# Kernel tuning notes

Hardware: AMD Instinct MI355X
Metric: run time of the kernel (lower is better)

## Reference

```python
import jax, jax.numpy as jnp
import numpy as np

N_NODES = 100000


def gcn_conv(x, edge_index, W, b, num_nodes):
    """PyG GCNConv: y = D^{-1/2} (A + I) D^{-1/2} (x W) + b.

    edge_index[0] = source (row), edge_index[1] = target (col);
    messages flow source -> target with symmetric normalization.
    """
    # add self loops
    loop = jnp.arange(num_nodes, dtype=edge_index.dtype)
    row = jnp.concatenate([edge_index[0], loop])  # [E+N]
    col = jnp.concatenate([edge_index[1], loop])  # [E+N]

    xw = x @ W  # [N, F_out] -- tiny GEMM, done before gather

    # degree of target nodes (incl. self loops)
    ones = jnp.ones(col.shape[0], dtype=x.dtype)
    deg = jax.ops.segment_sum(ones, col, num_segments=num_nodes)  # [N]
    dis = jax.lax.rsqrt(jnp.maximum(deg, 1e-12))
    dis = jnp.where(deg > 0, dis, 0.0)

    norm = dis[row] * dis[col]  # [E+N]
    msg = xw[row] * norm[:, None]  # gather + scale, [E+N, F_out]
    out = jax.ops.segment_sum(msg, col, num_segments=num_nodes)  # scatter-add
    return out + b


def setup_inputs() -> dict:
    key = jax.random.key(0)
    k1, k2, k3, k4 = jax.random.split(key, 4)
    num_attr, hidden, num_classes = 128, 16, 8
    n_edges = 3200000
    x = jax.random.normal(k1, (N_NODES, num_attr), dtype=jnp.float32)
    edge_index = jax.random.randint(k2, (2, n_edges), 0, N_NODES, dtype=jnp.int64)
    W1 = jax.random.normal(k3, (num_attr, hidden), dtype=jnp.float32) / np.sqrt(num_attr)
    b1 = jnp.zeros((hidden,), dtype=jnp.float32)
    W2 = jax.random.normal(k4, (hidden, num_classes), dtype=jnp.float32) / np.sqrt(hidden)
    b2 = jnp.zeros((num_classes,), dtype=jnp.float32)
    return {"x": x, "edge_index": edge_index, "W1": W1, "b1": b1, "W2": W2, "b2": b2}


def reference(x, edge_index, W1, b1, W2, b2):
    h = gcn_conv(x, edge_index, W1, b1, N_NODES)
    h = jax.nn.relu(h)
    # dropout is identity in eval mode
    h = gcn_conv(h, edge_index, W2, b2, N_NODES)
    return jax.nn.sigmoid(h)  # [N, num_classes]
```

## Files before the change

### kernel.cpp

```cpp
#include <hip/hip_runtime.h>
#include <math.h>

static constexpr int FI = 128;
static constexpr int FH = 16;
static constexpr int FO = 8;

static constexpr int BIN_SHIFT = 8;
static constexpr int BIN_NODES = 256;
static constexpr int MAX_BINS  = 512;
static constexpr int CAPB      = 8832;
static constexpr int SCHUNK    = 4096;
static constexpr int SThreads  = 512;

__device__ __forceinline__ unsigned short f2bf(float x) {
    unsigned u = __float_as_uint(x);
    u += 0x7FFFu + ((u >> 16) & 1u);
    return (unsigned short)(u >> 16);
}
__device__ __forceinline__ float bflo(unsigned u) { return __uint_as_float(u << 16); }
__device__ __forceinline__ float bfhi(unsigned u) { return __uint_as_float(u & 0xFFFF0000u); }

struct SMemScatter {
    int lcnt[MAX_BINS];
    int lstart[MAX_BINS];
    int lcur[MAX_BINS];
    int gbase[MAX_BINS];
    int wsum[8];
    unsigned int   staged[SCHUNK];
    unsigned short sbin[SCHUNK];
};
struct SMemGemm { float sw[FI * FH]; };
union SMemU { SMemScatter s; SMemGemm g; };

__launch_bounds__(SThreads)
__global__ void k_scatter_gemm(const int* __restrict__ row, const int* __restrict__ col,
                               int* __restrict__ binCursor, unsigned int* __restrict__ binned,
                               const float* __restrict__ x, const float* __restrict__ W1,
                               unsigned short* __restrict__ xw1, int E, int nchunks, int N) {
    __shared__ SMemU sm;
    int t = threadIdx.x;

    if ((int)blockIdx.x >= nchunks) {
        for (int i = t; i < FI * FH; i += SThreads) sm.g.sw[i] = W1[i];
        __syncthreads();
        int nl = t >> 2;
        int f  = (t & 3) * 4;
        int n  = ((int)blockIdx.x - nchunks) * 128 + nl;
        if (n >= N) return;
        const float4* xr = (const float4*)(x + (size_t)n * FI);
        float a0 = 0.f, a1 = 0.f, a2 = 0.f, a3 = 0.f;
        #pragma unroll 8
        for (int kq = 0; kq < FI / 4; ++kq) {
            float4 xv = xr[kq];
            float4 w0 = *(const float4*)&sm.g.sw[(kq * 4 + 0) * FH + f];
            float4 w1 = *(const float4*)&sm.g.sw[(kq * 4 + 1) * FH + f];
            float4 w2 = *(const float4*)&sm.g.sw[(kq * 4 + 2) * FH + f];
            float4 w3 = *(const float4*)&sm.g.sw[(kq * 4 + 3) * FH + f];
            a0 = fmaf(xv.x, w0.x, a0); a1 = fmaf(xv.x, w0.y, a1);
            a2 = fmaf(xv.x, w0.z, a2); a3 = fmaf(xv.x, w0.w, a3);
            a0 = fmaf(xv.y, w1.x, a0); a1 = fmaf(xv.y, w1.y, a1);
            a2 = fmaf(xv.y, w1.z, a2); a3 = fmaf(xv.y, w1.w, a3);
            a0 = fmaf(xv.z, w2.x, a0); a1 = fmaf(xv.z, w2.y, a1);
            a2 = fmaf(xv.z, w2.z, a2); a3 = fmaf(xv.z, w2.w, a3);
            a0 = fmaf(xv.w, w3.x, a0); a1 = fmaf(xv.w, w3.y, a1);
            a2 = fmaf(xv.w, w3.z, a2); a3 = fmaf(xv.w, w3.w, a3);
        }
        unsigned w0 = (unsigned)f2bf(a0) | ((unsigned)f2bf(a1) << 16);
        unsigned w1 = (unsigned)f2bf(a2) | ((unsigned)f2bf(a3) << 16);
        *(uint2*)(xw1 + (size_t)n * FH + f) = make_uint2(w0, w1);
        return;
    }

    int base = blockIdx.x * SCHUNK;
    int end  = base + SCHUNK; if (end > E) end = E;
    int m = end - base;
    sm.s.lcnt[t] = 0;
    __syncthreads();

    int nv = m >> 2;
    const int4* c4 = (const int4*)(col + base);
    int4 creg[2];
    #pragma unroll
    for (int j = 0; j < 2; ++j) {
        int k = t + j * SThreads;
        if (k < nv) {
            creg[j] = c4[k];
            atomicAdd(&sm.s.lcnt[creg[j].x >> BIN_SHIFT], 1);
            atomicAdd(&sm.s.lcnt[creg[j].y >> BIN_SHIFT], 1);
            atomicAdd(&sm.s.lcnt[creg[j].z >> BIN_SHIFT], 1);
            atomicAdd(&sm.s.lcnt[creg[j].w >> BIN_SHIFT], 1);
        }
    }
    for (int i = base + (nv << 2) + t; i < end; i += SThreads)
        atomicAdd(&sm.s.lcnt[col[i] >> BIN_SHIFT], 1);
    __syncthreads();

    int v = sm.s.lcnt[t];
    int inc = v;
    #pragma unroll
    for (int d = 1; d < 64; d <<= 1) {
        int u = __shfl_up(inc, d, 64);
        if ((t & 63) >= d) inc += u;
    }
    if ((t & 63) == 63) sm.s.wsum[t >> 6] = inc;
    __syncthreads();
    if (t < 8) {
        int w = sm.s.wsum[t];
        #pragma unroll
        for (int d = 1; d < 8; d <<= 1) {
            int u = __shfl_up(w, d, 8);
            if (t >= d) w += u;
        }
        sm.s.wsum[t] = w;
    }
    __syncthreads();
    {
        int waveoff = (t >= 64) ? sm.s.wsum[(t >> 6) - 1] : 0;
        int ex = waveoff + inc - v;
        sm.s.lstart[t] = ex;
        sm.s.lcur[t]   = ex;
        sm.s.gbase[t]  = v ? atomicAdd(&binCursor[t], v) : 0;
    }
    __syncthreads();

    const int4* r4 = (const int4*)(row + base);
    #pragma unroll
    for (int j = 0; j < 2; ++j) {
        int k = t + j * SThreads;
        if (k < nv) {
            int4 r = r4[k];
            int cc[4] = {creg[j].x, creg[j].y, creg[j].z, creg[j].w};
            int rr[4] = {r.x, r.y, r.z, r.w};
            #pragma unroll
            for (int jj = 0; jj < 4; ++jj) {
                int b = cc[jj] >> BIN_SHIFT;
                int pos = atomicAdd(&sm.s.lcur[b], 1);
                sm.s.staged[pos] = (unsigned)rr[jj] | ((unsigned)(cc[jj] & (BIN_NODES - 1)) << 17);
                sm.s.sbin[pos] = (unsigned short)b;
            }
        }
    }
    for (int i = base + (nv << 2) + t; i < end; i += SThreads) {
        int c = col[i];
        int b = c >> BIN_SHIFT;
        int pos = atomicAdd(&sm.s.lcur[b], 1);
        sm.s.staged[pos] = (unsigned)row[i] | ((unsigned)(c & (BIN_NODES - 1)) << 17);
        sm.s.sbin[pos] = (unsigned short)b;
    }
    __syncthreads();

    for (int i = t; i < m; i += SThreads) {
        int b = sm.s.sbin[i];
        int off = sm.s.gbase[b] + (i - sm.s.lstart[b]);
        if (off < CAPB) binned[b * CAPB + off] = sm.s.staged[i];
    }
}

__launch_bounds__(BIN_NODES)
__global__ void k_refine(const int* __restrict__ binCursor, const unsigned int* __restrict__ binned,
                         int* __restrict__ srow, int* __restrict__ starts, int* __restrict__ ends,
                         float* __restrict__ dis, unsigned short* __restrict__ xw1, int N) {
    __shared__ unsigned char arr[CAPB];
    __shared__ int cnt[BIN_NODES];
    __shared__ int wsum[4];
    int t = threadIdx.x;
    int b = blockIdx.x;
    int s = b * CAPB;
    int m = binCursor[b];
    if (m > CAPB) m = CAPB;
    cnt[t] = 0;
    __syncthreads();

    int mm = m & ~3;
    for (int i0 = t * 4; i0 < mm; i0 += BIN_NODES * 4) {
        uint4 v = *(const uint4*)(binned + s + i0);
        arr[i0 + 0] = (unsigned char)atomicAdd(&cnt[v.x >> 17], 1);
        arr[i0 + 1] = (unsigned char)atomicAdd(&cnt[v.y >> 17], 1);
        arr[i0 + 2] = (unsigned char)atomicAdd(&cnt[v.z >> 17], 1);
        arr[i0 + 3] = (unsigned char)atomicAdd(&cnt[v.w >> 17], 1);
    }
    for (int i = mm + t; i < m; i += BIN_NODES)
        arr[i] = (unsigned char)atomicAdd(&cnt[binned[s + i] >> 17], 1);
    __syncthreads();

    int deg = cnt[t];
    int inc = deg;
    #pragma unroll
    for (int d = 1; d < 64; d <<= 1) {
        int u = __shfl_up(inc, d, 64);
        if ((t & 63) >= d) inc += u;
    }
    if ((t & 63) == 63) wsum[t >> 6] = inc;
    __syncthreads();
    if (t < 4) {
        int w = wsum[t];
        #pragma unroll
        for (int d = 1; d < 4; d <<= 1) {
            int u = __shfl_up(w, d, 4);
            if (t >= d) w += u;
        }
        wsum[t] = w;
    }
    __syncthreads();
    int waveoff = (t >= 64) ? wsum[(t >> 6) - 1] : 0;
    int excl = waveoff + inc - deg;

    int n = b * BIN_NODES + t;
    float dv = rsqrtf((float)(deg + 1));
    if (n < N) {
        starts[n] = s + excl;
        ends[n]   = s + excl + deg;
        dis[n]    = dv;
    }
    cnt[t] = excl;
    __syncthreads();

    for (int i0 = t * 4; i0 < mm; i0 += BIN_NODES * 4) {
        uint4 v = *(const uint4*)(binned + s + i0);
        srow[s + cnt[v.x >> 17] + arr[i0 + 0]] = v.x & 0x1FFFF;
        srow[s + cnt[v.y >> 17] + arr[i0 + 1]] = v.y & 0x1FFFF;
        srow[s + cnt[v.z >> 17] + arr[i0 + 2]] = v.z & 0x1FFFF;
        srow[s + cnt[v.w >> 17] + arr[i0 + 3]] = v.w & 0x1FFFF;
    }
    for (int i = mm + t; i < m; i += BIN_NODES) {
        unsigned v = binned[s + i];
        srow[s + cnt[v >> 17] + arr[i]] = v & 0x1FFFF;
    }

    if (n < N) {
        uint4* p = (uint4*)(xw1 + (size_t)n * FH);
        uint4 va = p[0], vb = p[1];
        unsigned* u = &va.x;
        #pragma unroll
        for (int k = 0; k < 4; ++k)
            u[k] = (unsigned)f2bf(bflo(u[k]) * dv) | ((unsigned)f2bf(bfhi(u[k]) * dv) << 16);
        unsigned* w = &vb.x;
        #pragma unroll
        for (int k = 0; k < 4; ++k)
            w[k] = (unsigned)f2bf(bflo(w[k]) * dv) | ((unsigned)f2bf(bfhi(w[k]) * dv) << 16);
        p[0] = va; p[1] = vb;
    }
}

__launch_bounds__(256)
__global__ void k_agg1(const int* __restrict__ starts, const int* __restrict__ ends,
                       const int* __restrict__ srow, const float* __restrict__ dis,
                       const unsigned short* __restrict__ xw1s, const float* __restrict__ W2,
                       const float* __restrict__ b1, unsigned short* __restrict__ xw2s, int N) {
    __shared__ float sw[FH * FO];
    __shared__ float sb[FH];
    int t = threadIdx.x;
    if (t < FH * FO) sw[t] = W2[t];
    if (t < FH) sb[t] = b1[t];
    __syncthreads();

    int n = blockIdx.x * 128 + (t >> 1);
    int h = t & 1;
    if (n >= N) return;
    float dn = dis[n];
    int s = starts[n], e = ends[n];
    const uint4* xq = (const uint4*)xw1s;

    uint4 sp = xq[(size_t)n * 2 + h];
    float acc[8];
    acc[0]=bflo(sp.x); acc[1]=bfhi(sp.x); acc[2]=bflo(sp.y); acc[3]=bfhi(sp.y);
    acc[4]=bflo(sp.z); acc[5]=bfhi(sp.z); acc[6]=bflo(sp.w); acc[7]=bfhi(sp.w);

    int i = s;
    for (; i + 8 <= e; i += 8) {
        int rr[8];
        #pragma unroll
        for (int j = 0; j < 8; ++j) rr[j] = srow[i + j];
        uint4 pk[8];
        #pragma unroll
        for (int j = 0; j < 8; ++j) pk[j] = xq[(size_t)rr[j] * 2 + h];
        #pragma unroll
        for (int j = 0; j < 8; ++j) {
            acc[0]+=bflo(pk[j].x); acc[1]+=bfhi(pk[j].x);
            acc[2]+=bflo(pk[j].y); acc[3]+=bfhi(pk[j].y);
            acc[4]+=bflo(pk[j].z); acc[5]+=bfhi(pk[j].z);
            acc[6]+=bflo(pk[j].w); acc[7]+=bfhi(pk[j].w);
        }
    }
    for (; i < e; ++i) {
        uint4 p = xq[(size_t)srow[i] * 2 + h];
        acc[0]+=bflo(p.x); acc[1]+=bfhi(p.x);
        acc[2]+=bflo(p.y); acc[3]+=bfhi(p.y);
        acc[4]+=bflo(p.z); acc[5]+=bfhi(p.z);
        acc[6]+=bflo(p.w); acc[7]+=bfhi(p.w);
    }

    float hv[8];
    #pragma unroll
    for (int k = 0; k < 8; ++k) {
        float v = fmaf(dn, acc[k], sb[h * 8 + k]);
        hv[k] = v > 0.f ? v : 0.f;
    }
    float po[FO];
    #pragma unroll
    for (int o = 0; o < FO; ++o) {
        float a = 0.f;
        #pragma unroll
        for (int k = 0; k < 8; ++k) a = fmaf(hv[k], sw[(h * 8 + k) * FO + o], a);
        po[o] = a;
    }
    #pragma unroll
    for (int o = 0; o < FO; ++o) po[o] += __shfl_xor(po[o], 1, 64);
    int o0 = h * 4;
    unsigned w0 = (unsigned)f2bf(po[o0 + 0] * dn) | ((unsigned)f2bf(po[o0 + 1] * dn) << 16);
    unsigned w1 = (unsigned)f2bf(po[o0 + 2] * dn) | ((unsigned)f2bf(po[o0 + 3] * dn) << 16);
    *(uint2*)(xw2s + (size_t)n * FO + o0) = make_uint2(w0, w1);
}

__launch_bounds__(256)
__global__ void k_agg2(const int* __restrict__ starts, const int* __restrict__ ends,
                       const int* __restrict__ srow, const float* __restrict__ dis,
                       const unsigned short* __restrict__ xw2s, const float* __restrict__ b2,
                       float* __restrict__ out, int N) {
    int t = threadIdx.x;
    int n = blockIdx.x * 128 + (t >> 1);
    int h = t & 1;
    if (n >= N) return;
    float dn = dis[n];
    int s = starts[n], e = ends[n];
    const uint2* xq = (const uint2*)xw2s;

    uint2 sp = xq[(size_t)n * 2 + h];
    float acc[4];
    acc[0]=bflo(sp.x); acc[1]=bfhi(sp.x); acc[2]=bflo(sp.y); acc[3]=bfhi(sp.y);

    int i = s;
    for (; i + 8 <= e; i += 8) {
        int rr[8];
        #pragma unroll
        for (int j = 0; j < 8; ++j) rr[j] = srow[i + j];
        uint2 pk[8];
        #pragma unroll
        for (int j = 0; j < 8; ++j) pk[j] = xq[(size_t)rr[j] * 2 + h];
        #pragma unroll
        for (int j = 0; j < 8; ++j) {
            acc[0]+=bflo(pk[j].x); acc[1]+=bfhi(pk[j].x);
            acc[2]+=bflo(pk[j].y); acc[3]+=bfhi(pk[j].y);
        }
    }
    for (; i < e; ++i) {
        uint2 p = xq[(size_t)srow[i] * 2 + h];
        acc[0]+=bflo(p.x); acc[1]+=bfhi(p.x);
        acc[2]+=bflo(p.y); acc[3]+=bfhi(p.y);
    }

    int f0 = h * 4;
    float r[4];
    #pragma unroll
    for (int k = 0; k < 4; ++k) {
        float v = fmaf(dn, acc[k], b2[f0 + k]);
        r[k] = 1.f / (1.f + __expf(-v));
    }
    *(float4*)(out + (size_t)n * FO + f0) = make_float4(r[0], r[1], r[2], r[3]);
}

extern "C" void kernel_launch(void* const* d_in, const int* in_sizes, int n_in,
                              void* d_out, int out_size, void* d_ws, size_t ws_size,
                              hipStream_t stream) {
    const float* x  = (const float*)d_in[0];
    const int*   ei = (const int*)d_in[1];
    const float* W1 = (const float*)d_in[2];
    const float* b1 = (const float*)d_in[3];
    const float* W2 = (const float*)d_in[4];
    const float* b2 = (const float*)d_in[5];

    const int N = in_sizes[0] / FI;
    const int E = in_sizes[1] / 2;
    const int* row = ei;
    const int* col = ei + E;
    const int nbins = (N + BIN_NODES - 1) >> BIN_SHIFT;

    const int nchunks = (E + SCHUNK - 1) / SCHUNK;
    const int ngemm   = (N + 127) / 128;

    const size_t NP = 100352;
    const size_t BINSZ = (size_t)nbins * CAPB;
    float* base = (float*)d_ws;
    int*   starts    = (int*)base;
    int*   ends      = (int*)(base + NP);
    float* dis       = base + 2 * NP;
    int*   binCursor = (int*)(base + 3 * NP);
    unsigned int* binned = (unsigned int*)(base + 3 * NP + 1024);
    int*   srow      = (int*)(base + 3 * NP + 1024 + BINSZ);
    unsigned short* xw1s = (unsigned short*)(base + 3 * NP + 1024 + 2 * BINSZ);
    unsigned short* xw2s = (unsigned short*)(base + 3 * NP + 1024 + 2 * BINSZ + NP * 8);
    float* out = (float*)d_out;

    size_t needed = (3 * NP + 1024 + 2 * BINSZ + NP * 12) * 4;
    if (ws_size < needed) return;

    hipMemsetAsync(binCursor, 0, (size_t)nbins * sizeof(int), stream);
    k_scatter_gemm<<<nchunks + ngemm, SThreads, 0, stream>>>(row, col, binCursor, binned,
                                                             x, W1, xw1s, E, nchunks, N);
    k_refine      <<<nbins, BIN_NODES,          0, stream>>>(binCursor, binned, srow, starts, ends, dis, xw1s, N);
    k_agg1        <<<(2 * N + 255) / 256, 256,  0, stream>>>(starts, ends, srow, dis, xw1s, W2, b1, xw2s, N);
    k_agg2        <<<(2 * N + 255) / 256, 256,  0, stream>>>(starts, ends, srow, dis, xw2s, b2, out, N);
}
```

Before: 130.7 us.

## Reuse count-pass atomics for staging, widen chunks, pad CSR segments for int4 loads

The scatter kernel now processes 8192 edges per block and keeps the return value of the shared-memory counting atomic as each edge's local slot. This removes the second atomic pass over a separate cursor array. The bin id is split between a byte array and a spare bit in the staged word, which saves shared memory. The refine kernel pads each node's CSR segment start to a multiple of 4 so the aggregation kernels can fetch source indices with aligned int4 loads. The bin capacity grows to absorb the padding. The risks are larger per-block shared memory, which lowers occupancy, and a tighter usable bin capacity (CAPB-768) that could truncate edges in heavy bins.

```diff
diff --git a/kernel.cpp b/kernel.cpp
--- a/kernel.cpp
+++ b/kernel.cpp
@@ -8,8 +8,8 @@
 static constexpr int BIN_SHIFT = 8;
 static constexpr int BIN_NODES = 256;
 static constexpr int MAX_BINS  = 512;
-static constexpr int CAPB      = 8832;
-static constexpr int SCHUNK    = 4096;
+static constexpr int CAPB      = 9728;
+static constexpr int SCHUNK    = 8192;
 static constexpr int SThreads  = 512;
 
 __device__ __forceinline__ unsigned short f2bf(float x) {
@@ -23,16 +23,15 @@
 struct SMemScatter {
     int lcnt[MAX_BINS];
     int lstart[MAX_BINS];
-    int lcur[MAX_BINS];
     int gbase[MAX_BINS];
     int wsum[8];
-    unsigned int   staged[SCHUNK];
-    unsigned short sbin[SCHUNK];
+    unsigned int  staged[SCHUNK];
+    unsigned char sbin[SCHUNK];
 };
 struct SMemGemm { float sw[FI * FH]; };
 union SMemU { SMemScatter s; SMemGemm g; };
 
-__launch_bounds__(SThreads)
+__launch_bounds__(SThreads, 6)
 __global__ void k_scatter_gemm(const int* __restrict__ row, const int* __restrict__ col,
                                int* __restrict__ binCursor, unsigned int* __restrict__ binned,
                                const float* __restrict__ x, const float* __restrict__ W1,
@@ -65,9 +64,9 @@
             a0 = fmaf(xv.w, w3.x, a0); a1 = fmaf(xv.w, w3.y, a1);
             a2 = fmaf(xv.w, w3.z, a2); a3 = fmaf(xv.w, w3.w, a3);
         }
-        unsigned w0 = (unsigned)f2bf(a0) | ((unsigned)f2bf(a1) << 16);
-        unsigned w1 = (unsigned)f2bf(a2) | ((unsigned)f2bf(a3) << 16);
-        *(uint2*)(xw1 + (size_t)n * FH + f) = make_uint2(w0, w1);
+        unsigned p0 = (unsigned)f2bf(a0) | ((unsigned)f2bf(a1) << 16);
+        unsigned p1 = (unsigned)f2bf(a2) | ((unsigned)f2bf(a3) << 16);
+        *(uint2*)(xw1 + (size_t)n * FH + f) = make_uint2(p0, p1);
         return;
     }
 
@@ -79,20 +78,25 @@
 
     int nv = m >> 2;
     const int4* c4 = (const int4*)(col + base);
-    int4 creg[2];
-    #pragma unroll
-    for (int j = 0; j < 2; ++j) {
+    int4 creg[4];
+    unsigned short a16[16];
+    #pragma unroll
+    for (int j = 0; j < 4; ++j) {
         int k = t + j * SThreads;
         if (k < nv) {
             creg[j] = c4[k];
-            atomicAdd(&sm.s.lcnt[creg[j].x >> BIN_SHIFT], 1);
-            atomicAdd(&sm.s.lcnt[creg[j].y >> BIN_SHIFT], 1);
-            atomicAdd(&sm.s.lcnt[creg[j].z >> BIN_SHIFT], 1);
-            atomicAdd(&sm.s.lcnt[creg[j].w >> BIN_SHIFT], 1);
-        }
-    }
-    for (int i = base + (nv << 2) + t; i < end; i += SThreads)
-        atomicAdd(&sm.s.lcnt[col[i] >> BIN_SHIFT], 1);
+            a16[j*4+0] = (unsigned short)atomicAdd(&sm.s.lcnt[creg[j].x >> BIN_SHIFT], 1);
+            a16[j*4+1] = (unsigned short)atomicAdd(&sm.s.lcnt[creg[j].y >> BIN_SHIFT], 1);
+            a16[j*4+2] = (unsigned short)atomicAdd(&sm.s.lcnt[creg[j].z >> BIN_SHIFT], 1);
+            a16[j*4+3] = (unsigned short)atomicAdd(&sm.s.lcnt[creg[j].w >> BIN_SHIFT], 1);
+        }
+    }
+    int tailIdx = base + (nv << 2) + t;
+    int tailCol = 0, tailA = -1;
+    if (tailIdx < end) {
+        tailCol = col[tailIdx];
+        tailA = atomicAdd(&sm.s.lcnt[tailCol >> BIN_SHIFT], 1);
+    }
     __syncthreads();
 
     int v = sm.s.lcnt[t];
@@ -116,16 +120,14 @@
     __syncthreads();
     {
         int waveoff = (t >= 64) ? sm.s.wsum[(t >> 6) - 1] : 0;
-        int ex = waveoff + inc - v;
-        sm.s.lstart[t] = ex;
-        sm.s.lcur[t]   = ex;
+        sm.s.lstart[t] = waveoff + inc - v;
         sm.s.gbase[t]  = v ? atomicAdd(&binCursor[t], v) : 0;
     }
     __syncthreads();
 
     const int4* r4 = (const int4*)(row + base);
     #pragma unroll
-    for (int j = 0; j < 2; ++j) {
+    for (int j = 0; j < 4; ++j) {
         int k = t + j * SThreads;
         if (k < nv) {
             int4 r = r4[k];
@@ -134,25 +136,27 @@
             #pragma unroll
             for (int jj = 0; jj < 4; ++jj) {
                 int b = cc[jj] >> BIN_SHIFT;
-                int pos = atomicAdd(&sm.s.lcur[b], 1);
-                sm.s.staged[pos] = (unsigned)rr[jj] | ((unsigned)(cc[jj] & (BIN_NODES - 1)) << 17);
-                sm.s.sbin[pos] = (unsigned short)b;
+                int pos = sm.s.lstart[b] + a16[j*4+jj];
+                sm.s.staged[pos] = (unsigned)rr[jj] | ((unsigned)(cc[jj] & (BIN_NODES - 1)) << 17)
+                                 | ((unsigned)(b >> 8) << 25);
+                sm.s.sbin[pos] = (unsigned char)b;
             }
         }
     }
-    for (int i = base + (nv << 2) + t; i < end; i += SThreads) {
-        int c = col[i];
-        int b = c >> BIN_SHIFT;
-        int pos = atomicAdd(&sm.s.lcur[b], 1);
-        sm.s.staged[pos] = (unsigned)row[i] | ((unsigned)(c & (BIN_NODES - 1)) << 17);
-        sm.s.sbin[pos] = (unsigned short)b;
+    if (tailA >= 0) {
+        int b = tailCol >> BIN_SHIFT;
+        int pos = sm.s.lstart[b] + tailA;
+        sm.s.staged[pos] = (unsigned)row[tailIdx] | ((unsigned)(tailCol & (BIN_NODES - 1)) << 17)
+                         | ((unsigned)(b >> 8) << 25);
+        sm.s.sbin[pos] = (unsigned char)b;
     }
     __syncthreads();
 
     for (int i = t; i < m; i += SThreads) {
-        int b = sm.s.sbin[i];
+        unsigned sv = sm.s.staged[i];
+        int b = (int)sm.s.sbin[i] | (int)((sv >> 25) & 1u) << 8;
         int off = sm.s.gbase[b] + (i - sm.s.lstart[b]);
-        if (off < CAPB) binned[b * CAPB + off] = sm.s.staged[i];
+        if (off < CAPB) binned[b * CAPB + off] = sv & 0x1FFFFFFu;
     }
 }
 
@@ -167,7 +171,7 @@
     int b = blockIdx.x;
     int s = b * CAPB;
     int m = binCursor[b];
-    if (m > CAPB) m = CAPB;
+    if (m > CAPB - 768) m = CAPB - 768;
     cnt[t] = 0;
     __syncthreads();
 
@@ -183,8 +187,9 @@
         arr[i] = (unsigned char)atomicAdd(&cnt[binned[s + i] >> 17], 1);
     __syncthreads();
 
-    int deg = cnt[t];
-    int inc = deg;
+    int deg  = cnt[t];
+    int pdeg = (deg + 3) & ~3;
+    int inc = pdeg;
     #pragma unroll
     for (int d = 1; d < 64; d <<= 1) {
         int u = __shfl_up(inc, d, 64);
@@ -203,16 +208,16 @@
     }
     __syncthreads();
     int waveoff = (t >= 64) ? wsum[(t >> 6) - 1] : 0;
-    int excl = waveoff + inc - deg;
+    int pexcl = waveoff + inc - pdeg;
 
     int n = b * BIN_NODES + t;
     float dv = rsqrtf((float)(deg + 1));
     if (n < N) {
-        starts[n] = s + excl;
-        ends[n]   = s + excl + deg;
+        starts[n] = s + pexcl;
+        ends[n]   = s + pexcl + deg;
         dis[n]    = dv;
     }
-    cnt[t] = excl;
+    cnt[t] = pexcl;
     __syncthreads();
 
     for (int i0 = t * 4; i0 < mm; i0 += BIN_NODES * 4) {
@@ -268,12 +273,13 @@
 
     int i = s;
     for (; i + 8 <= e; i += 8) {
-        int rr[8];
-        #pragma unroll
-        for (int j = 0; j < 8; ++j) rr[j] = srow[i + j];
+        int4 ra = *(const int4*)(srow + i);
+        int4 rb = *(const int4*)(srow + i + 4);
         uint4 pk[8];
-        #pragma unroll
-        for (int j = 0; j < 8; ++j) pk[j] = xq[(size_t)rr[j] * 2 + h];
+        pk[0] = xq[(size_t)ra.x * 2 + h]; pk[1] = xq[(size_t)ra.y * 2 + h];
+        pk[2] = xq[(size_t)ra.z * 2 + h]; pk[3] = xq[(size_t)ra.w * 2 + h];
+        pk[4] = xq[(size_t)rb.x * 2 + h]; pk[5] = xq[(size_t)rb.y * 2 + h];
+        pk[6] = xq[(size_t)rb.z * 2 + h]; pk[7] = xq[(size_t)rb.w * 2 + h];
         #pragma unroll
         for (int j = 0; j < 8; ++j) {
             acc[0]+=bflo(pk[j].x); acc[1]+=bfhi(pk[j].x);
@@ -331,12 +337,13 @@
 
     int i = s;
     for (; i + 8 <= e; i += 8) {
-        int rr[8];
-        #pragma unroll
-        for (int j = 0; j < 8; ++j) rr[j] = srow[i + j];
+        int4 ra = *(const int4*)(srow + i);
+        int4 rb = *(const int4*)(srow + i + 4);
         uint2 pk[8];
-        #pragma unroll
-        for (int j = 0; j < 8; ++j) pk[j] = xq[(size_t)rr[j] * 2 + h];
+        pk[0] = xq[(size_t)ra.x * 2 + h]; pk[1] = xq[(size_t)ra.y * 2 + h];
+        pk[2] = xq[(size_t)ra.z * 2 + h]; pk[3] = xq[(size_t)ra.w * 2 + h];
+        pk[4] = xq[(size_t)rb.x * 2 + h]; pk[5] = xq[(size_t)rb.y * 2 + h];
+        pk[6] = xq[(size_t)rb.z * 2 + h]; pk[7] = xq[(size_t)rb.w * 2 + h];
         #pragma unroll
         for (int j = 0; j < 8; ++j) {
             acc[0]+=bflo(pk[j].x); acc[1]+=bfhi(pk[j].x);
```

New measurement: 116.9 us. 1.12x faster.
